# Optimization experiments

Hardware: AMD Instinct MI355X
Metric: run time of the kernel (lower is better)

The kernel has to match this reference:

```python
import jax, jax.numpy as jnp
import numpy as np

N_NODES = 50000
N_EDGES = 800000
NUM_GRAPHS = 64
EPS = 1e-5


def setup_inputs() -> dict:
    key = jax.random.key(0)
    ks = jax.random.split(key, 24)
    d = {}
    d['x'] = jax.random.normal(ks[0], (N_NODES, 128), dtype=jnp.float32)
    d['edge_index'] = jax.random.randint(ks[1], (2, N_EDGES), 0, N_NODES, dtype=jnp.int32)
    d['batch'] = jnp.sort(jax.random.randint(ks[2], (N_NODES,), 0, NUM_GRAPHS, dtype=jnp.int32))
    def w(k, shape, fan_in):
        return jax.random.normal(k, shape, dtype=jnp.float32) * (1.0 / np.sqrt(fan_in))
    d['W1'] = w(ks[3], (128, 256), 128)
    d['asrc1'] = w(ks[4], (4, 64), 64)
    d['adst1'] = w(ks[5], (4, 64), 64)
    d['b1'] = jnp.zeros((256,), jnp.float32)
    d['g1'] = jnp.ones((256,), jnp.float32)
    d['be1'] = jnp.zeros((256,), jnp.float32)
    d['W2'] = w(ks[6], (256, 256), 256)
    d['asrc2'] = w(ks[7], (4, 64), 64)
    d['adst2'] = w(ks[8], (4, 64), 64)
    d['b2'] = jnp.zeros((256,), jnp.float32)
    d['g2'] = jnp.ones((256,), jnp.float32)
    d['be2'] = jnp.zeros((256,), jnp.float32)
    d['W3'] = w(ks[9], (256, 128), 256)
    d['asrc3'] = w(ks[10], (1, 128), 128)
    d['adst3'] = w(ks[11], (1, 128), 128)
    d['b3'] = jnp.zeros((128,), jnp.float32)
    d['g3'] = jnp.ones((128,), jnp.float32)
    d['be3'] = jnp.zeros((128,), jnp.float32)
    d['Wp'] = w(ks[12], (256, 128), 256)
    d['bp'] = jnp.zeros((128,), jnp.float32)
    return d


def _gat(x, src, dst, W, a_src, a_dst, b, concat):
    # PyG GATConv: shared linear, per-edge additive attention, segment softmax over dst
    N = x.shape[0]
    H, C = a_src.shape
    xl = (x @ W).reshape(N, H, C)                       # [N,H,C]
    a_l = jnp.sum(xl * a_src[None], axis=-1)            # [N,H]
    a_r = jnp.sum(xl * a_dst[None], axis=-1)            # [N,H]
    e = jax.nn.leaky_relu(a_l[src] + a_r[dst], 0.2)     # [E,H]
    m = jax.ops.segment_max(e, dst, num_segments=N)
    m = jnp.where(jnp.isfinite(m), m, 0.0)
    p = jnp.exp(e - m[dst])
    s = jax.ops.segment_sum(p, dst, num_segments=N)
    alpha = p / (s[dst] + 1e-16)                        # [E,H]
    out = jax.ops.segment_sum(alpha[:, :, None] * xl[src], dst, num_segments=N)  # [N,H,C]
    out = out.reshape(N, H * C) if concat else out.mean(axis=1)
    return out + b


def _ln(x, g, b):
    mu = x.mean(-1, keepdims=True)
    var = x.var(-1, keepdims=True)
    return (x - mu) * jax.lax.rsqrt(var + EPS) * g + b


def reference(x, edge_index, batch, W1, asrc1, adst1, b1, g1, be1,
              W2, asrc2, adst2, b2, g2, be2,
              W3, asrc3, adst3, b3, g3, be3, Wp, bp):
    N = x.shape[0]
    loops = jnp.arange(N, dtype=edge_index.dtype)
    src = jnp.concatenate([edge_index[0], loops])  # add_self_loops=True
    dst = jnp.concatenate([edge_index[1], loops])
    h = jax.nn.relu(_ln(_gat(x, src, dst, W1, asrc1, adst1, b1, True), g1, be1))
    h = jax.nn.relu(_ln(_gat(h, src, dst, W2, asrc2, adst2, b2, True), g2, be2))
    h = jax.nn.relu(_ln(_gat(h, src, dst, W3, asrc3, adst3, b3, False), g3, be3))
    cnt = jax.ops.segment_sum(jnp.ones((N,), h.dtype), batch, num_segments=NUM_GRAPHS)
    h_mean = jax.ops.segment_sum(h, batch, num_segments=NUM_GRAPHS) / jnp.maximum(cnt, 1.0)[:, None]
    h_max = jax.ops.segment_max(h, batch, num_segments=NUM_GRAPHS)
    g = jnp.concatenate([h_mean, h_max], axis=-1)       # [B, 2*embed]
    return g @ Wp + bp
```

## Files before the change

### kernel.cpp

```cpp
#include <hip/hip_runtime.h>

#define EPS_LN 1e-5f
typedef unsigned int uint;

using bf16x8 = __attribute__((ext_vector_type(8))) short;
using f32x4  = __attribute__((ext_vector_type(4))) float;

__device__ inline float bf2f(ushort h){ return __uint_as_float(((uint)h) << 16); }
__device__ inline ushort f2bf(float f){
  uint u = __float_as_uint(f);
  u += 0x7fffu + ((u >> 16) & 1u);
  return (ushort)(u >> 16);
}

__global__ void k_deg(const int* __restrict__ ei, int* __restrict__ deg, int E, int N){
  int e = blockIdx.x * 256 + threadIdx.x;
  if (e >= E + N) return;
  int dst = (e < E) ? ei[E + e] : (e - E);
  atomicAdd(&deg[dst], 1);
}

__global__ __launch_bounds__(1024) void k_bsum(const int* __restrict__ deg, int* __restrict__ bsum, int n){
  __shared__ int ws[16];
  const int t = (int)threadIdx.x, lane = t & 63, w = t >> 6;
  int i = blockIdx.x * 1024 + t;
  int v = (i < n) ? deg[i] : 0;
  #pragma unroll
  for (int off = 32; off; off >>= 1) v += __shfl_xor(v, off);
  if (lane == 0) ws[w] = v;
  __syncthreads();
  if (t == 0){
    int s = 0;
    #pragma unroll
    for (int k = 0; k < 16; k++) s += ws[k];
    bsum[blockIdx.x] = s;
  }
}

__global__ __launch_bounds__(256) void k_misc(int* __restrict__ bsum, int nb,
                                              const int* __restrict__ batch, int* __restrict__ pos,
                                              int N, int G){
  const int t = (int)threadIdx.x;
  if (blockIdx.x == 0){
    if (t >= 64) return;
    const int lane = t;
    int carry = 0;
    for (int b0 = 0; b0 < nb; b0 += 64){
      int i = b0 + lane;
      int v = (i < nb) ? bsum[i] : 0;
      int s = v;
      #pragma unroll
      for (int off = 1; off < 64; off <<= 1){ int u = __shfl_up(s, off); if (lane >= off) s += u; }
      if (i < nb) bsum[i] = s - v + carry;
      carry += __shfl(s, 63);
    }
  } else {
    int g = t;
    if (g > G) return;
    int lo = 0, hi = N;
    while (lo < hi){
      int mid = (lo + hi) >> 1;
      if (batch[mid] < g) lo = mid + 1; else hi = mid;
    }
    pos[g] = lo;
  }
}

__global__ __launch_bounds__(1024) void k_scan2(const int* __restrict__ deg, const int* __restrict__ bpre,
                                                int* __restrict__ row_ptr, int* __restrict__ cursor, int n){
  __shared__ int wsum[16];
  const int t = (int)threadIdx.x, lane = t & 63, w = t >> 6;
  int i = blockIdx.x * 1024 + t;
  int v = (i < n) ? deg[i] : 0;
  int s = v;
  #pragma unroll
  for (int off = 1; off < 64; off <<= 1){ int u = __shfl_up(s, off); if (lane >= off) s += u; }
  if (lane == 63) wsum[w] = s;
  __syncthreads();
  if (w == 0 && lane < 16){
    int sc = wsum[lane];
    #pragma unroll
    for (int off = 1; off < 16; off <<= 1){ int u = __shfl_up(sc, off); if (lane >= off) sc += u; }
    wsum[lane] = sc;
  }
  __syncthreads();
  int prefix = bpre[blockIdx.x] + (w ? wsum[w - 1] : 0) + s;
  if (i < n){ row_ptr[i + 1] = prefix; cursor[i] = prefix - v; }
  if (i == 0) row_ptr[0] = 0;
}

__global__ void k_scatter(const int* __restrict__ ei, int* __restrict__ cursor,
                          int* __restrict__ csr_src, int E, int N){
  int e = blockIdx.x * 256 + threadIdx.x;
  if (e >= E + N) return;
  int src, dst;
  if (e < E){ src = ei[e]; dst = ei[E + e]; } else { src = dst = e - E; }
  int pos = atomicAdd(&cursor[dst], 1);
  csr_src[pos] = src;
}

__global__ void k_prep(const float* __restrict__ x, ushort* __restrict__ x_bf,
                       const float* __restrict__ W1, ushort* __restrict__ W1t,
                       const float* __restrict__ W2, ushort* __restrict__ W2t,
                       const float* __restrict__ W3, ushort* __restrict__ W3t, int N){
  int i = blockIdx.x * 256 + threadIdx.x;
  const int c0 = N * 32;
  if (i < c0){
    float4 v = reinterpret_cast<const float4*>(x)[i];
    ushort4 o; o.x = f2bf(v.x); o.y = f2bf(v.y); o.z = f2bf(v.z); o.w = f2bf(v.w);
    reinterpret_cast<ushort4*>(x_bf)[i] = o;
    return;
  }
  i -= c0;
  if (i < 256 * 128){
    int n = i >> 7, k = i & 127;
    W1t[i] = f2bf(W1[(size_t)k * 256 + n]);
    return;
  }
  i -= 256 * 128;
  if (i < 256 * 256){
    int n = i >> 8, k = i & 255;
    W2t[i] = f2bf(W2[(size_t)k * 256 + n]);
    return;
  }
  i -= 256 * 256;
  if (i < 128 * 256){
    int n = i >> 8, k = i & 255;
    W3t[i] = f2bf(W3[(size_t)k * 128 + n]);
  }
}

template<int K, int N, int H>
__global__ __launch_bounds__(256, 2) void k_mm(const ushort* __restrict__ A,
                                               const ushort* __restrict__ Wt,
                                               ushort* __restrict__ out,
                                               const float* __restrict__ asrc,
                                               const float* __restrict__ adst,
                                               float* __restrict__ al, float* __restrict__ ar,
                                               int M)
{
  constexpr int BANDS = (N / H) / 64;
  __shared__ __align__(16) ushort ldsA[128 * 128];
  __shared__ __align__(16) ushort ldsB[128 * 128];

  const int t = (int)threadIdx.x;
  const int lane = t & 63;
  const int w = t >> 6;
  const int wm = w >> 1, wn = w & 1;
  const int row0 = blockIdx.x * 128;
  const int n0 = blockIdx.y * 128;
  const int trow = t >> 4;
  const int tk = t & 15;

  f32x4 acc[4][4];
  #pragma unroll
  for (int mt = 0; mt < 4; mt++)
    #pragma unroll
    for (int nt = 0; nt < 4; nt++)
      acc[mt][nt] = (f32x4){0.f, 0.f, 0.f, 0.f};

  #pragma unroll
  for (int kt = 0; kt < K / 128; kt++){
    uint4 ra[8], rb[8];
    #pragma unroll
    for (int p = 0; p < 8; p++){
      int arow = p * 16 + trow;
      int grow = row0 + arow; if (grow > M - 1) grow = M - 1;
      ra[p] = *reinterpret_cast<const uint4*>(&A[(size_t)grow * K + kt * 128 + tk * 8]);
      rb[p] = *reinterpret_cast<const uint4*>(&Wt[(size_t)(n0 + arow) * K + kt * 128 + tk * 8]);
    }
    if (kt) __syncthreads();
    #pragma unroll
    for (int p = 0; p < 8; p++){
      int arow = p * 16 + trow;
      int sw = (tk ^ (arow & 7)) * 8;
      *reinterpret_cast<uint4*>(&ldsA[arow * 128 + sw]) = ra[p];
      *reinterpret_cast<uint4*>(&ldsB[arow * 128 + sw]) = rb[p];
    }
    __syncthreads();

    #pragma unroll
    for (int ks = 0; ks < 4; ks++){
      bf16x8 af[4], bfr[4];
      const int kb8 = ks * 4 + (lane >> 4);
      #pragma unroll
      for (int mt = 0; mt < 4; mt++){
        int arow = wm * 64 + mt * 16 + (lane & 15);
        af[mt] = *reinterpret_cast<const bf16x8*>(&ldsA[arow * 128 + ((kb8 ^ (arow & 7)) * 8)]);
        int brow = wn * 64 + mt * 16 + (lane & 15);
        bfr[mt] = *reinterpret_cast<const bf16x8*>(&ldsB[brow * 128 + ((kb8 ^ (brow & 7)) * 8)]);
      }
      #pragma unroll
      for (int mt = 0; mt < 4; mt++)
        #pragma unroll
        for (int nt = 0; nt < 4; nt++)
          acc[mt][nt] = __builtin_amdgcn_mfma_f32_16x16x32_bf16(af[mt], bfr[nt], acc[mt][nt], 0, 0, 0);
    }
  }

  #pragma unroll
  for (int mt = 0; mt < 4; mt++){
    const int grow_b = row0 + wm * 64 + mt * 16 + (lane >> 4) * 4;
    #pragma unroll
    for (int nt = 0; nt < 4; nt++){
      const int gcol = n0 + wn * 64 + nt * 16 + (lane & 15);
      #pragma unroll
      for (int r = 0; r < 4; r++){
        int grow = grow_b + r;
        if (grow < M) out[(size_t)grow * N + gcol] = f2bf(acc[mt][nt][r]);
      }
    }
  }

  float av[4], bv[4];
  #pragma unroll
  for (int nt = 0; nt < 4; nt++){
    int col = n0 + wn * 64 + nt * 16 + (lane & 15);
    av[nt] = asrc[col]; bv[nt] = adst[col];
  }
  float paA[4][4], pbA[4][4];
  #pragma unroll
  for (int mt = 0; mt < 4; mt++){
    #pragma unroll
    for (int r = 0; r < 4; r++){
      float pa = acc[mt][0][r] * av[0] + acc[mt][1][r] * av[1]
               + acc[mt][2][r] * av[2] + acc[mt][3][r] * av[3];
      float pb = acc[mt][0][r] * bv[0] + acc[mt][1][r] * bv[1]
               + acc[mt][2][r] * bv[2] + acc[mt][3][r] * bv[3];
      #pragma unroll
      for (int off = 1; off < 16; off <<= 1){ pa += __shfl_xor(pa, off); pb += __shfl_xor(pb, off); }
      paA[mt][r] = pa; pbA[mt][r] = pb;
    }
  }
  if constexpr (BANDS == 1){
    const int h = (n0 + wn * 64) / (N / H);
    if ((lane & 15) == 0){
      #pragma unroll
      for (int mt = 0; mt < 4; mt++){
        #pragma unroll
        for (int r = 0; r < 4; r++){
          int row = row0 + wm * 64 + mt * 16 + (lane >> 4) * 4 + r;
          if (row < M){
            al[(size_t)row * H + h] = paA[mt][r];
            ar[(size_t)row * H + h] = pbA[mt][r];
          }
        }
      }
    }
  } else {
    __syncthreads();
    float* fl = reinterpret_cast<float*>(ldsA);
    if (wn == 0 && (lane & 15) == 0){
      #pragma unroll
      for (int mt = 0; mt < 4; mt++){
        #pragma unroll
        for (int r = 0; r < 4; r++){
          int rl = wm * 64 + mt * 16 + (lane >> 4) * 4 + r;
          fl[rl] = paA[mt][r]; fl[128 + rl] = pbA[mt][r];
        }
      }
    }
    __syncthreads();
    if (wn == 1 && (lane & 15) == 0){
      #pragma unroll
      for (int mt = 0; mt < 4; mt++){
        #pragma unroll
        for (int r = 0; r < 4; r++){
          int rl = wm * 64 + mt * 16 + (lane >> 4) * 4 + r;
          int row = row0 + rl;
          if (row < M){
            al[row] = fl[rl] + paA[mt][r];
            ar[row] = fl[128 + rl] + pbA[mt][r];
          }
        }
      }
    }
  }
}

template<int DIM>
__device__ inline void gstep4(const char* __restrict__ xlb, int laneB, int s, float p, float* acc){
  uint2 v = *reinterpret_cast<const uint2*>(xlb + (size_t)((uint)s * (uint)(DIM * 2)) + laneB);
  acc[0] = fmaf(p, __uint_as_float(v.x << 16), acc[0]);
  acc[1] = fmaf(p, __uint_as_float(v.x & 0xffff0000u), acc[1]);
  acc[2] = fmaf(p, __uint_as_float(v.y << 16), acc[2]);
  acc[3] = fmaf(p, __uint_as_float(v.y & 0xffff0000u), acc[3]);
}
template<int DIM>
__device__ inline void gstep2(const char* __restrict__ xlb, int laneB, int s, float p, float* acc){
  uint v = *reinterpret_cast<const uint*>(xlb + (size_t)((uint)s * (uint)(DIM * 2)) + laneB);
  acc[0] = fmaf(p, __uint_as_float(v << 16), acc[0]);
  acc[1] = fmaf(p, __uint_as_float(v & 0xffff0000u), acc[1]);
}

template<int H, int DIM, bool BF16_OUT>
__global__ __launch_bounds__(256) void k_aggw(
    const ushort* __restrict__ xl,
    const float* __restrict__ al, const float* __restrict__ ar,
    const int* __restrict__ row_ptr, const int* __restrict__ csr_src,
    const float* __restrict__ bias, const float* __restrict__ gamma, const float* __restrict__ beta,
    float* __restrict__ out, int N)
{
  constexpr int EPL = DIM / 64;
  constexpr int PST = 68;
  const int tid = (int)threadIdx.x;
  const int wid = tid >> 6, lane = tid & 63;
  __shared__ float plds_all[4][H * PST];
  __shared__ int   slds_all[4][64];
  float* plds = plds_all[wid];
  int*   slds = slds_all[wid];
  const int n = blockIdx.x * 4 + wid;
  if (n >= N) return;
  const int start = __builtin_amdgcn_readfirstlane(row_ptr[n]);
  const int end   = __builtin_amdgcn_readfirstlane(row_ptr[n + 1]);
  const int deg   = end - start;
  const int hm    = (H == 4) ? (lane >> 4) : 0;
  const int hb    = hm * PST;
  const int laneB = lane * (EPL * 2);

  float arv[H];
  #pragma unroll
  for (int h = 0; h < H; h++) arv[h] = ar[(size_t)n * H + h];

  float acc[EPL];
  #pragma unroll
  for (int e = 0; e < EPL; e++) acc[e] = 0.f;
  float psum[H];
  const char* xlb = (const char*)xl;

  auto gather = [&](int cnt){
    int j = 0;
    for (; j + 8 <= cnt; j += 8){
      int s0 = slds[j+0], s1 = slds[j+1], s2 = slds[j+2], s3 = slds[j+3];
      int s4 = slds[j+4], s5 = slds[j+5], s6 = slds[j+6], s7 = slds[j+7];
      float q0 = plds[hb+j+0], q1 = plds[hb+j+1], q2 = plds[hb+j+2], q3 = plds[hb+j+3];
      float q4 = plds[hb+j+4], q5 = plds[hb+j+5], q6 = plds[hb+j+6], q7 = plds[hb+j+7];
      if constexpr (EPL == 4){
        gstep4<DIM>(xlb, laneB, s0, q0, acc); gstep4<DIM>(xlb, laneB, s1, q1, acc);
        gstep4<DIM>(xlb, laneB, s2, q2, acc); gstep4<DIM>(xlb, laneB, s3, q3, acc);
        gstep4<DIM>(xlb, laneB, s4, q4, acc); gstep4<DIM>(xlb, laneB, s5, q5, acc);
        gstep4<DIM>(xlb, laneB, s6, q6, acc); gstep4<DIM>(xlb, laneB, s7, q7, acc);
      } else {
        gstep2<DIM>(xlb, laneB, s0, q0, acc); gstep2<DIM>(xlb, laneB, s1, q1, acc);
        gstep2<DIM>(xlb, laneB, s2, q2, acc); gstep2<DIM>(xlb, laneB, s3, q3, acc);
        gstep2<DIM>(xlb, laneB, s4, q4, acc); gstep2<DIM>(xlb, laneB, s5, q5, acc);
        gstep2<DIM>(xlb, laneB, s6, q6, acc); gstep2<DIM>(xlb, laneB, s7, q7, acc);
      }
    }
    for (; j + 2 <= cnt; j += 2){
      int s0 = slds[j+0], s1 = slds[j+1];
      float q0 = plds[hb+j+0], q1 = plds[hb+j+1];
      if constexpr (EPL == 4){ gstep4<DIM>(xlb, laneB, s0, q0, acc); gstep4<DIM>(xlb, laneB, s1, q1, acc); }
      else                   { gstep2<DIM>(xlb, laneB, s0, q0, acc); gstep2<DIM>(xlb, laneB, s1, q1, acc); }
    }
    if (j < cnt){
      int s0 = slds[j];
      float q0 = plds[hb+j];
      if constexpr (EPL == 4) gstep4<DIM>(xlb, laneB, s0, q0, acc);
      else                    gstep2<DIM>(xlb, laneB, s0, q0, acc);
    }
  };

  if (deg <= 64){
    int src = csr_src[start + (lane < deg ? lane : deg - 1)];
    slds[lane] = src;
    float e[H];
    if constexpr (H == 4){
      float4 a4 = *reinterpret_cast<const float4*>(&al[(size_t)src * 4]);
      e[0] = a4.x + arv[0]; e[1] = a4.y + arv[1]; e[2] = a4.z + arv[2]; e[3] = a4.w + arv[3];
    } else {
      e[0] = al[src] + arv[0];
    }
    #pragma unroll
    for (int h = 0; h < H; h++){
      e[h] = e[h] > 0.f ? e[h] : 0.2f * e[h];
      if (lane >= deg) e[h] = -1e30f;
    }
    float mx[H];
    #pragma unroll
    for (int h = 0; h < H; h++){
      mx[h] = e[h];
      #pragma unroll
      for (int off = 32; off; off >>= 1) mx[h] = fmaxf(mx[h], __shfl_xor(mx[h], off));
    }
    #pragma unroll
    for (int h = 0; h < H; h++){
      float p = (lane < deg) ? __expf(e[h] - mx[h]) : 0.f;
      plds[h * PST + lane] = p;
      psum[h] = p;
      #pragma unroll
      for (int off = 32; off; off >>= 1) psum[h] += __shfl_xor(psum[h], off);
    }
    __asm__ volatile("s_waitcnt lgkmcnt(0)" ::: "memory");
    __builtin_amdgcn_wave_barrier();
    gather(deg);
  } else {
    float mx[H];
    #pragma unroll
    for (int h = 0; h < H; h++) mx[h] = -1e30f;
    for (int i = start + lane; i < end; i += 64){
      int src = csr_src[i];
      if constexpr (H == 4){
        float4 a4 = *reinterpret_cast<const float4*>(&al[(size_t)src * 4]);
        float e0 = a4.x + arv[0]; e0 = e0 > 0.f ? e0 : 0.2f * e0; mx[0] = fmaxf(mx[0], e0);
        float e1 = a4.y + arv[1]; e1 = e1 > 0.f ? e1 : 0.2f * e1; mx[1] = fmaxf(mx[1], e1);
        float e2 = a4.z + arv[2]; e2 = e2 > 0.f ? e2 : 0.2f * e2; mx[2] = fmaxf(mx[2], e2);
        float e3 = a4.w + arv[3]; e3 = e3 > 0.f ? e3 : 0.2f * e3; mx[3] = fmaxf(mx[3], e3);
      } else {
        float e = al[src] + arv[0]; e = e > 0.f ? e : 0.2f * e; mx[0] = fmaxf(mx[0], e);
      }
    }
    #pragma unroll
    for (int h = 0; h < H; h++){
      #pragma unroll
      for (int off = 32; off; off >>= 1) mx[h] = fmaxf(mx[h], __shfl_xor(mx[h], off));
    }
    #pragma unroll
    for (int h = 0; h < H; h++) psum[h] = 0.f;
    for (int c0 = start; c0 < end; c0 += 64){
      const int cnt = min(64, end - c0);
      __asm__ volatile("s_waitcnt lgkmcnt(0)" ::: "memory");
      __builtin_amdgcn_wave_barrier();
      if (lane < cnt){
        int src = csr_src[c0 + lane];
        slds[lane] = src;
        if constexpr (H == 4){
          float4 a4 = *reinterpret_cast<const float4*>(&al[(size_t)src * 4]);
          float e0 = a4.x + arv[0]; e0 = e0 > 0.f ? e0 : 0.2f * e0; float p0 = __expf(e0 - mx[0]);
          float e1 = a4.y + arv[1]; e1 = e1 > 0.f ? e1 : 0.2f * e1; float p1 = __expf(e1 - mx[1]);
          float e2 = a4.z + arv[2]; e2 = e2 > 0.f ? e2 : 0.2f * e2; float p2 = __expf(e2 - mx[2]);
          float e3 = a4.w + arv[3]; e3 = e3 > 0.f ? e3 : 0.2f * e3; float p3 = __expf(e3 - mx[3]);
          plds[0 * PST + lane] = p0; plds[1 * PST + lane] = p1;
          plds[2 * PST + lane] = p2; plds[3 * PST + lane] = p3;
          psum[0] += p0; psum[1] += p1; psum[2] += p2; psum[3] += p3;
        } else {
          float e = al[src] + arv[0]; e = e > 0.f ? e : 0.2f * e; float p = __expf(e - mx[0]);
          plds[lane] = p; psum[0] += p;
        }
      }
      __asm__ volatile("s_waitcnt lgkmcnt(0)" ::: "memory");
      __builtin_amdgcn_wave_barrier();
      gather(cnt);
    }
    #pragma unroll
    for (int h = 0; h < H; h++){
      #pragma unroll
      for (int off = 32; off; off >>= 1) psum[h] += __shfl_xor(psum[h], off);
    }
  }

  float ssel;
  if constexpr (H == 4){
    ssel = (hm == 0) ? psum[0] : (hm == 1) ? psum[1] : (hm == 2) ? psum[2] : psum[3];
  } else {
    ssel = psum[0];
  }
  const float inv = 1.f / (ssel + 1e-16f);

  float v[EPL];
  if constexpr (EPL == 4){
    float4 bb = *reinterpret_cast<const float4*>(&bias[lane * 4]);
    v[0] = fmaf(acc[0], inv, bb.x); v[1] = fmaf(acc[1], inv, bb.y);
    v[2] = fmaf(acc[2], inv, bb.z); v[3] = fmaf(acc[3], inv, bb.w);
  } else {
    float2 bb = *reinterpret_cast<const float2*>(&bias[lane * 2]);
    v[0] = fmaf(acc[0], inv, bb.x); v[1] = fmaf(acc[1], inv, bb.y);
  }
  float s1 = 0.f, s2 = 0.f;
  #pragma unroll
  for (int e = 0; e < EPL; e++){ s1 += v[e]; s2 += v[e] * v[e]; }
  #pragma unroll
  for (int off = 32; off; off >>= 1){ s1 += __shfl_xor(s1, off); s2 += __shfl_xor(s2, off); }
  const float mu = s1 / DIM;
  const float rstd = rsqrtf(s2 / DIM - mu * mu + EPS_LN);

  if constexpr (EPL == 4){
    float4 gg = *reinterpret_cast<const float4*>(&gamma[lane * 4]);
    float4 be = *reinterpret_cast<const float4*>(&beta[lane * 4]);
    float o0 = fmaxf((v[0] - mu) * rstd * gg.x + be.x, 0.f);
    float o1 = fmaxf((v[1] - mu) * rstd * gg.y + be.y, 0.f);
    float o2 = fmaxf((v[2] - mu) * rstd * gg.z + be.z, 0.f);
    float o3 = fmaxf((v[3] - mu) * rstd * gg.w + be.w, 0.f);
    if constexpr (BF16_OUT){
      uint2 pk;
      pk.x = (uint)f2bf(o0) | ((uint)f2bf(o1) << 16);
      pk.y = (uint)f2bf(o2) | ((uint)f2bf(o3) << 16);
      *reinterpret_cast<uint2*>(&reinterpret_cast<ushort*>(out)[(size_t)n * DIM + lane * 4]) = pk;
    } else {
      *reinterpret_cast<float4*>(&out[(size_t)n * DIM + lane * 4]) = make_float4(o0, o1, o2, o3);
    }
  } else {
    float2 gg = *reinterpret_cast<const float2*>(&gamma[lane * 2]);
    float2 be = *reinterpret_cast<const float2*>(&beta[lane * 2]);
    float o0 = fmaxf((v[0] - mu) * rstd * gg.x + be.x, 0.f);
    float o1 = fmaxf((v[1] - mu) * rstd * gg.y + be.y, 0.f);
    if constexpr (BF16_OUT){
      uint pk = (uint)f2bf(o0) | ((uint)f2bf(o1) << 16);
      reinterpret_cast<uint*>(out)[(size_t)n * (DIM / 2) + lane] = pk;
    } else {
      *reinterpret_cast<float2*>(&out[(size_t)n * DIM + lane * 2]) = make_float2(o0, o1);
    }
  }
}

__global__ __launch_bounds__(128) void k_pool(const float* __restrict__ h, const int* __restrict__ pos,
    float* __restrict__ pool_sum, unsigned* __restrict__ pool_max){
  const int c = (int)threadIdx.x;
  const int g = blockIdx.x >> 2;
  const int q = blockIdx.x & 3;
  const int s = pos[g], e = pos[g + 1];
  const int len = e - s;
  if (len <= 0) return;
  const int chunk = (len + 3) >> 2;
  const int n0 = s + q * chunk;
  const int n1 = min(n0 + chunk, e);
  if (n0 >= n1) return;
  float sum = 0.f, mx = 0.f;
  for (int n = n0; n < n1; n++){
    float v = h[(size_t)n * 128 + c];
    sum += v; mx = fmaxf(mx, v);
  }
  atomicAdd(&pool_sum[g * 128 + c], sum);
  atomicMax(&pool_max[g * 128 + c], __float_as_uint(mx));
}

__global__ __launch_bounds__(128) void k_final(const float* __restrict__ pool_sum,
    const unsigned* __restrict__ pool_max, const int* __restrict__ pos,
    const float* __restrict__ Wp, const float* __restrict__ bp, float* __restrict__ out){
  const int g = blockIdx.x;
  const int j = (int)threadIdx.x;
  float inv = 1.f / fmaxf((float)(pos[g + 1] - pos[g]), 1.f);
  float acc = bp[j];
  #pragma unroll 4
  for (int k = 0; k < 128; k++)
    acc = fmaf(pool_sum[g * 128 + k] * inv, Wp[k * 128 + j], acc);
  #pragma unroll 4
  for (int k = 0; k < 128; k++)
    acc = fmaf(__uint_as_float(pool_max[g * 128 + k]), Wp[(128 + k) * 128 + j], acc);
  out[g * 128 + j] = acc;
}

extern "C" void kernel_launch(void* const* d_in, const int* in_sizes, int n_in,
                              void* d_out, int out_size, void* d_ws, size_t ws_size,
                              hipStream_t stream){
  const float* x     = (const float*)d_in[0];
  const int*   ei    = (const int*)d_in[1];
  const int*   batch = (const int*)d_in[2];
  const float* W1    = (const float*)d_in[3];
  const float* asrc1 = (const float*)d_in[4];
  const float* adst1 = (const float*)d_in[5];
  const float* b1    = (const float*)d_in[6];
  const float* g1    = (const float*)d_in[7];
  const float* be1   = (const float*)d_in[8];
  const float* W2    = (const float*)d_in[9];
  const float* asrc2 = (const float*)d_in[10];
  const float* adst2 = (const float*)d_in[11];
  const float* b2    = (const float*)d_in[12];
  const float* g2    = (const float*)d_in[13];
  const float* be2   = (const float*)d_in[14];
  const float* W3    = (const float*)d_in[15];
  const float* asrc3 = (const float*)d_in[16];
  const float* adst3 = (const float*)d_in[17];
  const float* b3    = (const float*)d_in[18];
  const float* g3    = (const float*)d_in[19];
  const float* be3   = (const float*)d_in[20];
  const float* Wp    = (const float*)d_in[21];
  const float* bp    = (const float*)d_in[22];

  const int N = in_sizes[0] / 128;
  const int E = in_sizes[1] / 2;
  const int G = out_size / 128;
  const int EN = E + N;

  char* ws = (char*)d_ws;
  size_t off = 0;
  auto alloc = [&](size_t bytes) -> char* {
    char* p = ws + off;
    off = (off + bytes + 255) & ~(size_t)255;
    return p;
  };
  ushort*   region0  = (ushort*)alloc((size_t)N * 256 * 2);
  ushort*   x_bf     = region0;
  ushort*   h_bf     = region0;
  ushort*   xbufA    = (ushort*)alloc((size_t)N * 256 * 2);
  float*    xbufB    = (float*)alloc((size_t)N * 128 * 4);
  float*    al       = (float*)alloc((size_t)N * 4 * 4);
  float*    ar       = (float*)alloc((size_t)N * 4 * 4);
  int*      deg      = (int*)alloc((size_t)N * 4);
  int*      row_ptr  = (int*)alloc((size_t)(N + 1) * 4);
  int*      cursor   = (int*)alloc((size_t)N * 4);
  int*      csr_src  = (int*)alloc((size_t)EN * 4);
  int*      pos      = (int*)alloc((size_t)(G + 1) * 4);
  float*    pool_sum = (float*)alloc((size_t)G * 128 * 4);
  unsigned* pool_max = (unsigned*)alloc((size_t)G * 128 * 4);
  ushort*   W1t      = (ushort*)alloc((size_t)256 * 128 * 2);
  ushort*   W2t      = (ushort*)alloc((size_t)256 * 256 * 2);
  ushort*   W3t      = (ushort*)alloc((size_t)128 * 256 * 2);
  const int NB = (N + 1023) / 1024;
  int*      bsum     = (int*)alloc((size_t)NB * 4);

  hipMemsetAsync(deg, 0, (size_t)N * 4, stream);
  hipMemsetAsync(pool_sum, 0, (size_t)G * 128 * 4, stream);
  hipMemsetAsync(pool_max, 0, (size_t)G * 128 * 4, stream);

  k_deg<<<(EN + 255) / 256, 256, 0, stream>>>(ei, deg, E, N);
  k_bsum<<<NB, 1024, 0, stream>>>(deg, bsum, N);
  k_misc<<<2, 256, 0, stream>>>(bsum, NB, batch, pos, N, G);
  k_scan2<<<NB, 1024, 0, stream>>>(deg, bsum, row_ptr, cursor, N);
  k_scatter<<<(EN + 255) / 256, 256, 0, stream>>>(ei, cursor, csr_src, E, N);
  {
    int total = N * 32 + 256 * 128 + 256 * 256 + 128 * 256;
    k_prep<<<(total + 255) / 256, 256, 0, stream>>>(x, x_bf, W1, W1t, W2, W2t, W3, W3t, N);
  }

  const int MB = (N + 127) / 128;
  const int NB4 = (N + 3) / 4;

  k_mm<128, 256, 4><<<dim3(MB, 2), 256, 0, stream>>>(x_bf, W1t, xbufA, asrc1, adst1, al, ar, N);
  k_aggw<4, 256, true><<<NB4, 256, 0, stream>>>(xbufA, al, ar, row_ptr, csr_src, b1, g1, be1, (float*)h_bf, N);

  k_mm<256, 256, 4><<<dim3(MB, 2), 256, 0, stream>>>(h_bf, W2t, xbufA, asrc2, adst2, al, ar, N);
  k_aggw<4, 256, true><<<NB4, 256, 0, stream>>>(xbufA, al, ar, row_ptr, csr_src, b2, g2, be2, (float*)h_bf, N);

  k_mm<256, 128, 1><<<dim3(MB, 1), 256, 0, stream>>>(h_bf, W3t, xbufA, asrc3, adst3, al, ar, N);
  k_aggw<1, 128, false><<<NB4, 256, 0, stream>>>(xbufA, al, ar, row_ptr, csr_src, b3, g3, be3, xbufB, N);

  k_pool<<<G * 4, 128, 0, stream>>>(xbufB, pos, pool_sum, pool_max);
  k_final<<<G, 128, 0, stream>>>(pool_sum, pool_max, pos, Wp, bp, (float*)d_out);
}
```

Baseline: 462.5 us.

## Split GAT aggregation into alpha, column-sliced SpMM, and LayerNorm kernels

Attention coefficients are now computed once per edge in a separate kernel and stored as bf16 per head. The projected features are written by the GEMM in a column-sliced layout, so the SpMM kernel gathers narrow contiguous slices per source node, improving cache locality of the random gathers. Bias is added in the SpMM and LayerNorm+ReLU moves to its own kernel. This adds extra global traffic for alpha and the intermediate buffer, plus more kernel launches.

After: 982.4 us. 2.12x slower.

```diff
diff --git a/kernel.cpp b/kernel.cpp
--- a/kernel.cpp
+++ b/kernel.cpp
@@ -130,16 +130,17 @@
   }
 }
 
-template<int K, int N, int H>
+template<int K, int N, int H, int SC>
 __global__ __launch_bounds__(256, 2) void k_mm(const ushort* __restrict__ A,
                                                const ushort* __restrict__ Wt,
-                                               ushort* __restrict__ out,
+                                               ushort* __restrict__ xls,
                                                const float* __restrict__ asrc,
                                                const float* __restrict__ adst,
                                                float* __restrict__ al, float* __restrict__ ar,
                                                int M)
 {
   constexpr int BANDS = (N / H) / 64;
+  constexpr int LOG2SC = (SC == 32) ? 5 : 4;
   __shared__ __align__(16) ushort ldsA[128 * 128];
   __shared__ __align__(16) ushort ldsB[128 * 128];
 
@@ -204,10 +205,11 @@
     #pragma unroll
     for (int nt = 0; nt < 4; nt++){
       const int gcol = n0 + wn * 64 + nt * 16 + (lane & 15);
+      const size_t sbase = ((size_t)(gcol >> LOG2SC) * M) * SC + (gcol & (SC - 1));
       #pragma unroll
       for (int r = 0; r < 4; r++){
         int grow = grow_b + r;
-        if (grow < M) out[(size_t)grow * N + gcol] = f2bf(acc[mt][nt][r]);
+        if (grow < M) xls[sbase + (size_t)grow * SC] = f2bf(acc[mt][nt][r]);
       }
     }
   }
@@ -278,92 +280,25 @@
   }
 }
 
-template<int DIM>
-__device__ inline void gstep4(const char* __restrict__ xlb, int laneB, int s, float p, float* acc){
-  uint2 v = *reinterpret_cast<const uint2*>(xlb + (size_t)((uint)s * (uint)(DIM * 2)) + laneB);
-  acc[0] = fmaf(p, __uint_as_float(v.x << 16), acc[0]);
-  acc[1] = fmaf(p, __uint_as_float(v.x & 0xffff0000u), acc[1]);
-  acc[2] = fmaf(p, __uint_as_float(v.y << 16), acc[2]);
-  acc[3] = fmaf(p, __uint_as_float(v.y & 0xffff0000u), acc[3]);
-}
-template<int DIM>
-__device__ inline void gstep2(const char* __restrict__ xlb, int laneB, int s, float p, float* acc){
-  uint v = *reinterpret_cast<const uint*>(xlb + (size_t)((uint)s * (uint)(DIM * 2)) + laneB);
-  acc[0] = fmaf(p, __uint_as_float(v << 16), acc[0]);
-  acc[1] = fmaf(p, __uint_as_float(v & 0xffff0000u), acc[1]);
-}
-
-template<int H, int DIM, bool BF16_OUT>
-__global__ __launch_bounds__(256) void k_aggw(
-    const ushort* __restrict__ xl,
+template<int H>
+__global__ __launch_bounds__(256) void k_alpha(
     const float* __restrict__ al, const float* __restrict__ ar,
     const int* __restrict__ row_ptr, const int* __restrict__ csr_src,
-    const float* __restrict__ bias, const float* __restrict__ gamma, const float* __restrict__ beta,
-    float* __restrict__ out, int N)
+    ushort* __restrict__ alpha, int N, int EN)
 {
-  constexpr int EPL = DIM / 64;
-  constexpr int PST = 68;
   const int tid = (int)threadIdx.x;
   const int wid = tid >> 6, lane = tid & 63;
-  __shared__ float plds_all[4][H * PST];
-  __shared__ int   slds_all[4][64];
-  float* plds = plds_all[wid];
-  int*   slds = slds_all[wid];
   const int n = blockIdx.x * 4 + wid;
   if (n >= N) return;
-  const int start = __builtin_amdgcn_readfirstlane(row_ptr[n]);
-  const int end   = __builtin_amdgcn_readfirstlane(row_ptr[n + 1]);
-  const int deg   = end - start;
-  const int hm    = (H == 4) ? (lane >> 4) : 0;
-  const int hb    = hm * PST;
-  const int laneB = lane * (EPL * 2);
+  const int start = row_ptr[n], end = row_ptr[n + 1];
+  const int deg = end - start;
 
   float arv[H];
   #pragma unroll
   for (int h = 0; h < H; h++) arv[h] = ar[(size_t)n * H + h];
-
-  float acc[EPL];
-  #pragma unroll
-  for (int e = 0; e < EPL; e++) acc[e] = 0.f;
-  float psum[H];
-  const char* xlb = (const char*)xl;
-
-  auto gather = [&](int cnt){
-    int j = 0;
-    for (; j + 8 <= cnt; j += 8){
-      int s0 = slds[j+0], s1 = slds[j+1], s2 = slds[j+2], s3 = slds[j+3];
-      int s4 = slds[j+4], s5 = slds[j+5], s6 = slds[j+6], s7 = slds[j+7];
-      float q0 = plds[hb+j+0], q1 = plds[hb+j+1], q2 = plds[hb+j+2], q3 = plds[hb+j+3];
-      float q4 = plds[hb+j+4], q5 = plds[hb+j+5], q6 = plds[hb+j+6], q7 = plds[hb+j+7];
-      if constexpr (EPL == 4){
-        gstep4<DIM>(xlb, laneB, s0, q0, acc); gstep4<DIM>(xlb, laneB, s1, q1, acc);
-        gstep4<DIM>(xlb, laneB, s2, q2, acc); gstep4<DIM>(xlb, laneB, s3, q3, acc);
-        gstep4<DIM>(xlb, laneB, s4, q4, acc); gstep4<DIM>(xlb, laneB, s5, q5, acc);
-        gstep4<DIM>(xlb, laneB, s6, q6, acc); gstep4<DIM>(xlb, laneB, s7, q7, acc);
-      } else {
-        gstep2<DIM>(xlb, laneB, s0, q0, acc); gstep2<DIM>(xlb, laneB, s1, q1, acc);
-        gstep2<DIM>(xlb, laneB, s2, q2, acc); gstep2<DIM>(xlb, laneB, s3, q3, acc);
-        gstep2<DIM>(xlb, laneB, s4, q4, acc); gstep2<DIM>(xlb, laneB, s5, q5, acc);
-        gstep2<DIM>(xlb, laneB, s6, q6, acc); gstep2<DIM>(xlb, laneB, s7, q7, acc);
-      }
-    }
-    for (; j + 2 <= cnt; j += 2){
-      int s0 = slds[j+0], s1 = slds[j+1];
-      float q0 = plds[hb+j+0], q1 = plds[hb+j+1];
-      if constexpr (EPL == 4){ gstep4<DIM>(xlb, laneB, s0, q0, acc); gstep4<DIM>(xlb, laneB, s1, q1, acc); }
-      else                   { gstep2<DIM>(xlb, laneB, s0, q0, acc); gstep2<DIM>(xlb, laneB, s1, q1, acc); }
-    }
-    if (j < cnt){
-      int s0 = slds[j];
-      float q0 = plds[hb+j];
-      if constexpr (EPL == 4) gstep4<DIM>(xlb, laneB, s0, q0, acc);
-      else                    gstep2<DIM>(xlb, laneB, s0, q0, acc);
-    }
-  };
 
   if (deg <= 64){
     int src = csr_src[start + (lane < deg ? lane : deg - 1)];
-    slds[lane] = src;
     float e[H];
     if constexpr (H == 4){
       float4 a4 = *reinterpret_cast<const float4*>(&al[(size_t)src * 4]);
@@ -371,29 +306,25 @@
     } else {
       e[0] = al[src] + arv[0];
     }
+    float p[H], inv[H];
     #pragma unroll
     for (int h = 0; h < H; h++){
       e[h] = e[h] > 0.f ? e[h] : 0.2f * e[h];
       if (lane >= deg) e[h] = -1e30f;
-    }
-    float mx[H];
-    #pragma unroll
-    for (int h = 0; h < H; h++){
-      mx[h] = e[h];
-      #pragma unroll
-      for (int off = 32; off; off >>= 1) mx[h] = fmaxf(mx[h], __shfl_xor(mx[h], off));
-    }
-    #pragma unroll
-    for (int h = 0; h < H; h++){
-      float p = (lane < deg) ? __expf(e[h] - mx[h]) : 0.f;
-      plds[h * PST + lane] = p;
-      psum[h] = p;
-      #pragma unroll
-      for (int off = 32; off; off >>= 1) psum[h] += __shfl_xor(psum[h], off);
-    }
-    __asm__ volatile("s_waitcnt lgkmcnt(0)" ::: "memory");
-    __builtin_amdgcn_wave_barrier();
-    gather(deg);
+      float mx = e[h];
+      #pragma unroll
+      for (int off = 32; off; off >>= 1) mx = fmaxf(mx, __shfl_xor(mx, off));
+      p[h] = (lane < deg) ? __expf(e[h] - mx) : 0.f;
+      float s = p[h];
+      #pragma unroll
+      for (int off = 32; off; off >>= 1) s += __shfl_xor(s, off);
+      inv[h] = 1.f / (s + 1e-16f);
+    }
+    if (lane < deg){
+      #pragma unroll
+      for (int h = 0; h < H; h++)
+        alpha[(size_t)h * EN + start + lane] = f2bf(p[h] * inv[h]);
+    }
   } else {
     float mx[H];
     #pragma unroll
@@ -415,56 +346,124 @@
       #pragma unroll
       for (int off = 32; off; off >>= 1) mx[h] = fmaxf(mx[h], __shfl_xor(mx[h], off));
     }
-    #pragma unroll
-    for (int h = 0; h < H; h++) psum[h] = 0.f;
-    for (int c0 = start; c0 < end; c0 += 64){
-      const int cnt = min(64, end - c0);
-      __asm__ volatile("s_waitcnt lgkmcnt(0)" ::: "memory");
-      __builtin_amdgcn_wave_barrier();
-      if (lane < cnt){
-        int src = csr_src[c0 + lane];
-        slds[lane] = src;
-        if constexpr (H == 4){
-          float4 a4 = *reinterpret_cast<const float4*>(&al[(size_t)src * 4]);
-          float e0 = a4.x + arv[0]; e0 = e0 > 0.f ? e0 : 0.2f * e0; float p0 = __expf(e0 - mx[0]);
-          float e1 = a4.y + arv[1]; e1 = e1 > 0.f ? e1 : 0.2f * e1; float p1 = __expf(e1 - mx[1]);
-          float e2 = a4.z + arv[2]; e2 = e2 > 0.f ? e2 : 0.2f * e2; float p2 = __expf(e2 - mx[2]);
-          float e3 = a4.w + arv[3]; e3 = e3 > 0.f ? e3 : 0.2f * e3; float p3 = __expf(e3 - mx[3]);
-          plds[0 * PST + lane] = p0; plds[1 * PST + lane] = p1;
-          plds[2 * PST + lane] = p2; plds[3 * PST + lane] = p3;
-          psum[0] += p0; psum[1] += p1; psum[2] += p2; psum[3] += p3;
-        } else {
-          float e = al[src] + arv[0]; e = e > 0.f ? e : 0.2f * e; float p = __expf(e - mx[0]);
-          plds[lane] = p; psum[0] += p;
-        }
-      }
-      __asm__ volatile("s_waitcnt lgkmcnt(0)" ::: "memory");
-      __builtin_amdgcn_wave_barrier();
-      gather(cnt);
-    }
+    float ps[H];
+    #pragma unroll
+    for (int h = 0; h < H; h++) ps[h] = 0.f;
+    for (int i = start + lane; i < end; i += 64){
+      int src = csr_src[i];
+      if constexpr (H == 4){
+        float4 a4 = *reinterpret_cast<const float4*>(&al[(size_t)src * 4]);
+        float e0 = a4.x + arv[0]; e0 = e0 > 0.f ? e0 : 0.2f * e0; ps[0] += __expf(e0 - mx[0]);
+        float e1 = a4.y + arv[1]; e1 = e1 > 0.f ? e1 : 0.2f * e1; ps[1] += __expf(e1 - mx[1]);
+        float e2 = a4.z + arv[2]; e2 = e2 > 0.f ? e2 : 0.2f * e2; ps[2] += __expf(e2 - mx[2]);
+        float e3 = a4.w + arv[3]; e3 = e3 > 0.f ? e3 : 0.2f * e3; ps[3] += __expf(e3 - mx[3]);
+      } else {
+        float e = al[src] + arv[0]; e = e > 0.f ? e : 0.2f * e; ps[0] += __expf(e - mx[0]);
+      }
+    }
+    float inv[H];
     #pragma unroll
     for (int h = 0; h < H; h++){
       #pragma unroll
-      for (int off = 32; off; off >>= 1) psum[h] += __shfl_xor(psum[h], off);
-    }
-  }
-
-  float ssel;
-  if constexpr (H == 4){
-    ssel = (hm == 0) ? psum[0] : (hm == 1) ? psum[1] : (hm == 2) ? psum[2] : psum[3];
-  } else {
-    ssel = psum[0];
-  }
-  const float inv = 1.f / (ssel + 1e-16f);
-
+      for (int off = 32; off; off >>= 1) ps[h] += __shfl_xor(ps[h], off);
+      inv[h] = 1.f / (ps[h] + 1e-16f);
+    }
+    for (int i = start + lane; i < end; i += 64){
+      int src = csr_src[i];
+      if constexpr (H == 4){
+        float4 a4 = *reinterpret_cast<const float4*>(&al[(size_t)src * 4]);
+        float e0 = a4.x + arv[0]; e0 = e0 > 0.f ? e0 : 0.2f * e0;
+        float e1 = a4.y + arv[1]; e1 = e1 > 0.f ? e1 : 0.2f * e1;
+        float e2 = a4.z + arv[2]; e2 = e2 > 0.f ? e2 : 0.2f * e2;
+        float e3 = a4.w + arv[3]; e3 = e3 > 0.f ? e3 : 0.2f * e3;
+        alpha[(size_t)0 * EN + i] = f2bf(__expf(e0 - mx[0]) * inv[0]);
+        alpha[(size_t)1 * EN + i] = f2bf(__expf(e1 - mx[1]) * inv[1]);
+        alpha[(size_t)2 * EN + i] = f2bf(__expf(e2 - mx[2]) * inv[2]);
+        alpha[(size_t)3 * EN + i] = f2bf(__expf(e3 - mx[3]) * inv[3]);
+      } else {
+        float e = al[src] + arv[0]; e = e > 0.f ? e : 0.2f * e;
+        alpha[i] = f2bf(__expf(e - mx[0]) * inv[0]);
+      }
+    }
+  }
+}
+
+template<int DIM, int SC, int H>
+__global__ __launch_bounds__(256) void k_spmm(
+    const ushort* __restrict__ xls,
+    const ushort* __restrict__ alpha,
+    const int* __restrict__ row_ptr, const int* __restrict__ csr_src,
+    const float* __restrict__ bias,
+    ushort* __restrict__ ybuf,
+    int N, int EN)
+{
+  constexpr int LPE = SC / 2;
+  constexpr int EG = 64 / LPE;
+  constexpr int NPW = 8;
+  const int tid = (int)threadIdx.x;
+  const int wid = tid >> 6, lane = tid & 63;
+  const int slice = blockIdx.x & 7;
+  const int chunk = blockIdx.x >> 3;
+  const int eg = lane / LPE, lc = lane % LPE;
+  const int h = (slice * SC * H) / DIM;
+  const ushort* xsl = xls + (size_t)slice * N * SC;
+  const ushort* alp = alpha + (size_t)h * EN;
+  const int colb = slice * SC + lc * 2;
+  const float b0 = bias[colb], b1 = bias[colb + 1];
+
+  const int n0 = chunk * (4 * NPW) + wid * NPW;
+  for (int k = 0; k < NPW; k++){
+    const int n = n0 + k;
+    if (n >= N) return;
+    const int start = row_ptr[n], end = row_ptr[n + 1];
+    float p0 = 0.f, p1 = 0.f, q0 = 0.f, q1 = 0.f;
+    int jA = start + eg, jB = start + EG + eg;
+    int sA = (jA < end) ? __builtin_nontemporal_load(&csr_src[jA]) : 0;
+    int sB = (jB < end) ? __builtin_nontemporal_load(&csr_src[jB]) : 0;
+    float aA = (jA < end) ? bf2f(__builtin_nontemporal_load(&alp[jA])) : 0.f;
+    float aB = (jB < end) ? bf2f(__builtin_nontemporal_load(&alp[jB])) : 0.f;
+    for (int j = start; j < end; j += 2 * EG){
+      const int jA2 = j + 2 * EG + eg, jB2 = j + 3 * EG + eg;
+      int sA2 = (jA2 < end) ? __builtin_nontemporal_load(&csr_src[jA2]) : 0;
+      int sB2 = (jB2 < end) ? __builtin_nontemporal_load(&csr_src[jB2]) : 0;
+      float aA2 = (jA2 < end) ? bf2f(__builtin_nontemporal_load(&alp[jA2])) : 0.f;
+      float aB2 = (jB2 < end) ? bf2f(__builtin_nontemporal_load(&alp[jB2])) : 0.f;
+      uint vA = *reinterpret_cast<const uint*>(&xsl[(size_t)sA * SC + lc * 2]);
+      uint vB = *reinterpret_cast<const uint*>(&xsl[(size_t)sB * SC + lc * 2]);
+      p0 = fmaf(aA, __uint_as_float(vA << 16), p0);
+      p1 = fmaf(aA, __uint_as_float(vA & 0xffff0000u), p1);
+      q0 = fmaf(aB, __uint_as_float(vB << 16), q0);
+      q1 = fmaf(aB, __uint_as_float(vB & 0xffff0000u), q1);
+      sA = sA2; sB = sB2; aA = aA2; aB = aB2;
+    }
+    float a0 = p0 + q0, a1 = p1 + q1;
+    #pragma unroll
+    for (int off = LPE; off < 64; off <<= 1){ a0 += __shfl_xor(a0, off); a1 += __shfl_xor(a1, off); }
+    if (lane < LPE){
+      uint pk = (uint)f2bf(a0 + b0) | ((uint)f2bf(a1 + b1) << 16);
+      __builtin_nontemporal_store(pk, reinterpret_cast<uint*>(&ybuf[(size_t)n * DIM + colb]));
+    }
+  }
+}
+
+template<int DIM, bool F32OUT>
+__global__ __launch_bounds__(256) void k_ln(const ushort* __restrict__ ybuf,
+    const float* __restrict__ gamma, const float* __restrict__ beta,
+    void* __restrict__ outp, int N)
+{
+  constexpr int EPL = DIM / 64;
+  const int tid = (int)threadIdx.x;
+  const int wid = tid >> 6, lane = tid & 63;
+  const int n = blockIdx.x * 4 + wid;
+  if (n >= N) return;
   float v[EPL];
   if constexpr (EPL == 4){
-    float4 bb = *reinterpret_cast<const float4*>(&bias[lane * 4]);
-    v[0] = fmaf(acc[0], inv, bb.x); v[1] = fmaf(acc[1], inv, bb.y);
-    v[2] = fmaf(acc[2], inv, bb.z); v[3] = fmaf(acc[3], inv, bb.w);
+    uint2 pv = *reinterpret_cast<const uint2*>(&ybuf[(size_t)n * DIM + lane * 4]);
+    v[0] = __uint_as_float(pv.x << 16); v[1] = __uint_as_float(pv.x & 0xffff0000u);
+    v[2] = __uint_as_float(pv.y << 16); v[3] = __uint_as_float(pv.y & 0xffff0000u);
   } else {
-    float2 bb = *reinterpret_cast<const float2*>(&bias[lane * 2]);
-    v[0] = fmaf(acc[0], inv, bb.x); v[1] = fmaf(acc[1], inv, bb.y);
+    uint pv = *reinterpret_cast<const uint*>(&ybuf[(size_t)n * DIM + lane * 2]);
+    v[0] = __uint_as_float(pv << 16); v[1] = __uint_as_float(pv & 0xffff0000u);
   }
   float s1 = 0.f, s2 = 0.f;
   #pragma unroll
@@ -481,24 +480,20 @@
     float o1 = fmaxf((v[1] - mu) * rstd * gg.y + be.y, 0.f);
     float o2 = fmaxf((v[2] - mu) * rstd * gg.z + be.z, 0.f);
     float o3 = fmaxf((v[3] - mu) * rstd * gg.w + be.w, 0.f);
-    if constexpr (BF16_OUT){
-      uint2 pk;
-      pk.x = (uint)f2bf(o0) | ((uint)f2bf(o1) << 16);
-      pk.y = (uint)f2bf(o2) | ((uint)f2bf(o3) << 16);
-      *reinterpret_cast<uint2*>(&reinterpret_cast<ushort*>(out)[(size_t)n * DIM + lane * 4]) = pk;
-    } else {
-      *reinterpret_cast<float4*>(&out[(size_t)n * DIM + lane * 4]) = make_float4(o0, o1, o2, o3);
-    }
+    uint2 pk;
+    pk.x = (uint)f2bf(o0) | ((uint)f2bf(o1) << 16);
+    pk.y = (uint)f2bf(o2) | ((uint)f2bf(o3) << 16);
+    *reinterpret_cast<uint2*>(&reinterpret_cast<ushort*>(outp)[(size_t)n * DIM + lane * 4]) = pk;
   } else {
     float2 gg = *reinterpret_cast<const float2*>(&gamma[lane * 2]);
     float2 be = *reinterpret_cast<const float2*>(&beta[lane * 2]);
     float o0 = fmaxf((v[0] - mu) * rstd * gg.x + be.x, 0.f);
     float o1 = fmaxf((v[1] - mu) * rstd * gg.y + be.y, 0.f);
-    if constexpr (BF16_OUT){
+    if constexpr (F32OUT){
+      *reinterpret_cast<float2*>(&reinterpret_cast<float*>(outp)[(size_t)n * DIM + lane * 2]) = make_float2(o0, o1);
+    } else {
       uint pk = (uint)f2bf(o0) | ((uint)f2bf(o1) << 16);
-      reinterpret_cast<uint*>(out)[(size_t)n * (DIM / 2) + lane] = pk;
-    } else {
-      *reinterpret_cast<float2*>(&out[(size_t)n * DIM + lane * 2]) = make_float2(o0, o1);
+      *reinterpret_cast<uint*>(&reinterpret_cast<ushort*>(outp)[(size_t)n * DIM + lane * 2]) = pk;
     }
   }
 }
@@ -582,7 +577,9 @@
   ushort*   region0  = (ushort*)alloc((size_t)N * 256 * 2);
   ushort*   x_bf     = region0;
   ushort*   h_bf     = region0;
-  ushort*   xbufA    = (ushort*)alloc((size_t)N * 256 * 2);
+  ushort*   xls      = (ushort*)alloc((size_t)N * 256 * 2);
+  ushort*   ybuf     = (ushort*)alloc((size_t)N * 256 * 2);
+  ushort*   alphaB   = (ushort*)alloc((size_t)4 * EN * 2);
   float*    xbufB    = (float*)alloc((size_t)N * 128 * 4);
   float*    al       = (float*)alloc((size_t)N * 4 * 4);
   float*    ar       = (float*)alloc((size_t)N * 4 * 4);
@@ -615,15 +612,22 @@
 
   const int MB = (N + 127) / 128;
   const int NB4 = (N + 3) / 4;
-
-  k_mm<128, 256, 4><<<dim3(MB, 2), 256, 0, stream>>>(x_bf, W1t, xbufA, asrc1, adst1, al, ar, N);
-  k_aggw<4, 256, true><<<NB4, 256, 0, stream>>>(xbufA, al, ar, row_ptr, csr_src, b1, g1, be1, (float*)h_bf, N);
-
-  k_mm<256, 256, 4><<<dim3(MB, 2), 256, 0, stream>>>(h_bf, W2t, xbufA, asrc2, adst2, al, ar, N);
-  k_aggw<4, 256, true><<<NB4, 256, 0, stream>>>(xbufA, al, ar, row_ptr, csr_src, b2, g2, be2, (float*)h_bf, N);
-
-  k_mm<256, 128, 1><<<dim3(MB, 1), 256, 0, stream>>>(h_bf, W3t, xbufA, asrc3, adst3, al, ar, N);
-  k_aggw<1, 128, false><<<NB4, 256, 0, stream>>>(xbufA, al, ar, row_ptr, csr_src, b3, g3, be3, xbufB, N);
+  const int NCH = ((N + 31) / 32) * 8;
+
+  k_mm<128, 256, 4, 32><<<dim3(MB, 2), 256, 0, stream>>>(x_bf, W1t, xls, asrc1, adst1, al, ar, N);
+  k_alpha<4><<<NB4, 256, 0, stream>>>(al, ar, row_ptr, csr_src, alphaB, N, EN);
+  k_spmm<256, 32, 4><<<NCH, 256, 0, stream>>>(xls, alphaB, row_ptr, csr_src, b1, ybuf, N, EN);
+  k_ln<256, false><<<NB4, 256, 0, stream>>>(ybuf, g1, be1, h_bf, N);
+
+  k_mm<256, 256, 4, 32><<<dim3(MB, 2), 256, 0, stream>>>(h_bf, W2t, xls, asrc2, adst2, al, ar, N);
+  k_alpha<4><<<NB4, 256, 0, stream>>>(al, ar, row_ptr, csr_src, alphaB, N, EN);
+  k_spmm<256, 32, 4><<<NCH, 256, 0, stream>>>(xls, alphaB, row_ptr, csr_src, b2, ybuf, N, EN);
+  k_ln<256, false><<<NB4, 256, 0, stream>>>(ybuf, g2, be2, h_bf, N);
+
+  k_mm<256, 128, 1, 16><<<dim3(MB, 1), 256, 0, stream>>>(h_bf, W3t, xls, asrc3, adst3, al, ar, N);
+  k_alpha<1><<<NB4, 256, 0, stream>>>(al, ar, row_ptr, csr_src, alphaB, N, EN);
+  k_spmm<128, 16, 1><<<NCH, 256, 0, stream>>>(xls, alphaB, row_ptr, csr_src, b3, ybuf, N, EN);
+  k_ln<128, true><<<NB4, 256, 0, stream>>>(ybuf, g3, be3, xbufB, N);
 
   k_pool<<<G * 4, 128, 0, stream>>>(xbufB, pos, pool_sum, pool_max);
   k_final<<<G, 128, 0, stream>>>(pool_sum, pool_max, pos, Wp, bp, (float*)d_out);
```
